# Performance work log

Measured on AMD Instinct MI355X. Metric: run time of the kernel, lower is better.

## Reference

```python
import jax, jax.numpy as jnp
import numpy as np

TEMPERATURE = 0.1
NORM_EPS = 1e-12   # F.normalize default eps
LOSS_EPS = 1e-6

def _l2norm_c(x):
    # L2-normalize along channel dim (axis=1), matching F.normalize(dim=1)
    n = jnp.sqrt(jnp.sum(x * x, axis=1, keepdims=True))
    return x / jnp.maximum(n, NORM_EPS)

def setup_inputs() -> dict:
    key = jax.random.key(0)
    k1, k2, k3 = jax.random.split(key, 3)
    N, C, H, W = 8, 64, 64, 64
    rgb_map = jax.random.normal(k1, (N, C, H, W), dtype=jnp.float32)
    ir_map = jax.random.normal(k2, (N, C, H, W), dtype=jnp.float32)
    targets = jax.random.randint(k3, (N,), 0, 2)  # unused by the forward math
    return {"rgb_map": rgb_map, "ir_map": ir_map, "targets": targets}

def reference(rgb_map, ir_map, targets):
    N, C, H, W = rgb_map.shape
    rgb = _l2norm_c(rgb_map).reshape(N, C, H * W)   # [N, C, P]
    ir = _l2norm_c(ir_map).reshape(N, C, H * W)     # [N, C, P]
    # [N, P, P] similarity, then temperature exp
    logit = jnp.exp(jnp.einsum('ncp,ncq->npq', rgb, ir) / TEMPERATURE)
    pos = jnp.trace(logit, axis1=1, axis2=2)        # diagonal (positive) sum per sample
    tot = jnp.sum(logit, axis=(-1, -2))             # full row/col sum per sample
    loss = -jnp.log(pos / (tot + LOSS_EPS)).mean()
    return loss
```

## Files before the change

kernel.cpp:

```cpp
#include <hip/hip_runtime.h>

#define N_ 8
#define C_ 64
#define P_ 4096

typedef float f32x4 __attribute__((ext_vector_type(4)));
typedef short bf16x8 __attribute__((ext_vector_type(8)));

__device__ __forceinline__ unsigned short f2bf(float f) {
  unsigned int u = __builtin_bit_cast(unsigned int, f);
  u = (u + 0x7fffu + ((u >> 16) & 1u)) >> 16;
  return (unsigned short)u;
}

__global__ void __launch_bounds__(256) norm_transpose(
    const float* __restrict__ rgb, const float* __restrict__ ir,
    unsigned short* __restrict__ rgbnT, unsigned short* __restrict__ irnT) {
  const int idx = blockIdx.x * 256 + threadIdx.x;
  const int n = idx >> 12;
  const int p = idx & (P_ - 1);
  const float* src = (blockIdx.y == 0) ? rgb : ir;
  unsigned short* dst = (blockIdx.y == 0) ? rgbnT : irnT;
  const float SC = 14.4269504088896340736f;
  const float* col = src + (size_t)n * C_ * P_ + p;
  float v[C_];
  float ss = 0.f;
#pragma unroll
  for (int c = 0; c < C_; ++c) {
    v[c] = col[(size_t)c * P_];
    ss += v[c] * v[c];
  }
  float inv = 1.0f / fmaxf(sqrtf(ss), 1e-12f);
  if (blockIdx.y == 0) inv *= SC;
  const int gx = (blockIdx.y == 0) ? 0 : (p & 7);
  unsigned short* o = dst + ((size_t)n * P_ + p) * C_;
#pragma unroll
  for (int g = 0; g < 8; ++g) {
    bf16x8 pack;
#pragma unroll
    for (int j = 0; j < 8; ++j) pack[j] = (short)f2bf(v[g * 8 + j] * inv);
    *reinterpret_cast<bf16x8*>(o + (g ^ gx) * 8) = pack;
  }
}

__device__ __forceinline__ void stage_tile(const unsigned short* src,
                                           unsigned short* dst, int tid,
                                           int wid) {
#pragma unroll
  for (int r = 0; r < 2; ++r) {
    __builtin_amdgcn_global_load_lds(
        (const __attribute__((address_space(1))) void*)(src +
                                                        (size_t)(r * 256 + tid) * 8),
        (__attribute__((address_space(3))) void*)(dst + (r * 256 + wid * 64) * 8),
        16, 0, 0);
  }
}

__global__ void __launch_bounds__(256) gemm_exp_reduce(
    const unsigned short* __restrict__ aT, const unsigned short* __restrict__ bT,
    float* __restrict__ partials) {
  const int lin = blockIdx.x;
  const int n = lin & 7;
  const int local = lin >> 3;
  const int pc = local & 15;
  const int qc = local >> 4;
  const int tid = threadIdx.x;
  const int lane = tid & 63;
  const int wid = tid >> 6;
  const int pbase = pc * 256 + wid * 64;
  const int q0 = qc * 512;
  const unsigned short* A = aT + (size_t)n * P_ * C_;
  const unsigned short* B = bT + (size_t)n * P_ * C_;
  const int r16 = lane & 15;
  const int kofs = (lane >> 4) * 8;

  __shared__ __align__(16) unsigned short bs0[64 * 64];
  __shared__ __align__(16) unsigned short bs1[64 * 64];
  __shared__ __align__(16) unsigned short bs2[64 * 64];
  __shared__ __align__(16) unsigned short bs3[64 * 64];

  bf16x8 af[2][4];
#pragma unroll
  for (int ks = 0; ks < 2; ++ks)
#pragma unroll
    for (int mi = 0; mi < 4; ++mi)
      af[ks][mi] = *reinterpret_cast<const bf16x8*>(
          A + (size_t)(pbase + mi * 16 + r16) * C_ + ks * 32 + kofs);

  stage_tile(B + (size_t)(q0 + 0 * 64) * C_, bs0, tid, wid);
  stage_tile(B + (size_t)(q0 + 1 * 64) * C_, bs1, tid, wid);
  stage_tile(B + (size_t)(q0 + 2 * 64) * C_, bs2, tid, wid);

  unsigned short *pcur = bs0, *pnx1 = bs1, *pnx2 = bs2, *pnx3 = bs3;

  const f32x4 zc = (f32x4)(0.f);
  float t0 = 0.f, t1 = 0.f, t2 = 0.f, t3 = 0.f, pos = 0.f;
  const int col = lane & 15;
  const int rowb = (lane >> 4) * 4;

  unsigned fragoff[2][4];
#pragma unroll
  for (int ks = 0; ks < 2; ++ks)
#pragma unroll
    for (int ni = 0; ni < 4; ++ni) {
      const int row = ni * 16 + r16;
      const int seg = ks * 4 + (lane >> 4);
      fragoff[ks][ni] = (unsigned)((row * 64 + ((seg ^ (lane & 7)) * 8)) * 2);
    }

#pragma unroll 1
  for (int t = 0; t < 8; ++t) {
    asm volatile("s_waitcnt vmcnt(4)" ::: "memory");
    __builtin_amdgcn_sched_barrier(0);
    __builtin_amdgcn_s_barrier();

    int s = t + 3;
    if (s >= 8) s -= 8;
    stage_tile(B + (size_t)(q0 + s * 64) * C_, pnx3, tid, wid);

    const unsigned bpa = (unsigned)(size_t)pcur;
    f32x4 braw[2][4];
#pragma unroll
    for (int ks = 0; ks < 2; ++ks)
#pragma unroll
      for (int ni = 0; ni < 4; ++ni) {
        const unsigned addr = bpa + fragoff[ks][ni];
        asm volatile("ds_read_b128 %0, %1"
                     : "=v"(braw[ks][ni])
                     : "v"(addr));
      }
    asm volatile("s_waitcnt lgkmcnt(0)" ::: "memory");
    __builtin_amdgcn_sched_barrier(0);

    f32x4 acc[4][4];
    __builtin_amdgcn_s_setprio(1);
#pragma unroll
    for (int mi = 0; mi < 4; ++mi)
#pragma unroll
      for (int ni = 0; ni < 4; ++ni)
        acc[mi][ni] = __builtin_amdgcn_mfma_f32_16x16x32_bf16(
            af[0][mi], __builtin_bit_cast(bf16x8, braw[0][ni]), zc, 0, 0, 0);
#pragma unroll
    for (int mi = 0; mi < 4; ++mi)
#pragma unroll
      for (int ni = 0; ni < 4; ++ni)
        acc[mi][ni] = __builtin_amdgcn_mfma_f32_16x16x32_bf16(
            af[1][mi], __builtin_bit_cast(bf16x8, braw[1][ni]), acc[mi][ni],
            0, 0, 0);
    __builtin_amdgcn_s_setprio(0);

#pragma unroll
    for (int mi = 0; mi < 4; ++mi)
#pragma unroll
      for (int ni = 0; ni < 4; ++ni) {
        const f32x4 v = acc[mi][ni];
        t0 += __builtin_amdgcn_exp2f(v[0]);
        t1 += __builtin_amdgcn_exp2f(v[1]);
        t2 += __builtin_amdgcn_exp2f(v[2]);
        t3 += __builtin_amdgcn_exp2f(v[3]);
      }
    const int qb = q0 + t * 64;
    if (pbase == qb) {
#pragma unroll
      for (int mi = 0; mi < 4; ++mi)
#pragma unroll
        for (int r = 0; r < 4; ++r)
          if (rowb + r == col) pos += __builtin_amdgcn_exp2f(acc[mi][mi][r]);
    }

    unsigned short* tmp = pcur;
    pcur = pnx1;
    pnx1 = pnx2;
    pnx2 = pnx3;
    pnx3 = tmp;
  }

  float tot = (t0 + t1) + (t2 + t3);
#pragma unroll
  for (int off = 32; off > 0; off >>= 1) {
    tot += __shfl_down(tot, off);
    pos += __shfl_down(pos, off);
  }
  __shared__ float sb[8];
  if (lane == 0) { sb[wid * 2] = pos; sb[wid * 2 + 1] = tot; }
  __syncthreads();
  if (tid == 0) {
    const float pp = sb[0] + sb[2] + sb[4] + sb[6];
    const float tt = sb[1] + sb[3] + sb[5] + sb[7];
    const int bid = n * 128 + pc * 8 + qc;
    partials[bid * 2] = pp;
    partials[bid * 2 + 1] = tt;
  }
}

__global__ void __launch_bounds__(1024) finalize(
    const float* __restrict__ partials, float* __restrict__ out) {
  const int tid = threadIdx.x;
  const int lane = tid & 63, wid = tid >> 6;
  __shared__ float sp[16], st[16], sl[8];
  const int n = tid >> 7;
  const int i = tid & 127;
  float p = partials[(n * 128 + i) * 2];
  float t = partials[(n * 128 + i) * 2 + 1];
#pragma unroll
  for (int off = 32; off > 0; off >>= 1) {
    p += __shfl_down(p, off);
    t += __shfl_down(t, off);
  }
  if (lane == 0) { sp[wid] = p; st[wid] = t; }
  __syncthreads();
  if (tid < 8) {
    const float pp = sp[2 * tid] + sp[2 * tid + 1];
    const float tt = st[2 * tid] + st[2 * tid + 1];
    sl[tid] = -logf(pp / (tt + 1e-6f));
  }
  __syncthreads();
  if (tid == 0) {
    float loss = 0.f;
#pragma unroll
    for (int k = 0; k < 8; ++k) loss += sl[k];
    out[0] = loss * (1.0f / N_);
  }
}

extern "C" void kernel_launch(void* const* d_in, const int* in_sizes, int n_in,
                              void* d_out, int out_size, void* d_ws, size_t ws_size,
                              hipStream_t stream) {
  const float* rgb = (const float*)d_in[0];
  const float* ir = (const float*)d_in[1];
  float* out = (float*)d_out;

  unsigned short* rgbnT = (unsigned short*)d_ws;
  unsigned short* irnT = rgbnT + (size_t)N_ * P_ * C_;
  float* partials = (float*)(irnT + (size_t)N_ * P_ * C_);

  dim3 g1(N_ * P_ / 256, 2);
  norm_transpose<<<g1, 256, 0, stream>>>(rgb, ir, rgbnT, irnT);

  gemm_exp_reduce<<<1024, 256, 0, stream>>>(rgbnT, irnT, partials);

  finalize<<<1, 1024, 0, stream>>>(partials, out);
}
```

Measured before the change: 41.47 us.

## Give each wave private double-buffered B tiles and drop block barriers

Each wave now stages its own copy of every 64-row B tile into a private double buffer in LDS, so the per-iteration block-wide s_barrier and the shared 4-deep ring are removed. The next tile's load is issued into the current buffer right after its fragments are read into registers. Each wave also writes its own partial sums, which removes the final shared-memory reduction and __syncthreads, and finalize sums four times as many partials. The cost is four times the global/L2 traffic for B and twice the LDS footprint, with only a 2-deep prefetch.

```diff
diff --git a/kernel.cpp b/kernel.cpp
--- a/kernel.cpp
+++ b/kernel.cpp
@@ -43,16 +43,15 @@
   }
 }
 
-__device__ __forceinline__ void stage_tile(const unsigned short* src,
-                                           unsigned short* dst, int tid,
-                                           int wid) {
-#pragma unroll
-  for (int r = 0; r < 2; ++r) {
+__device__ __forceinline__ void stage_tile_wave(const unsigned short* src,
+                                                unsigned short* dst,
+                                                int lane) {
+#pragma unroll
+  for (int r = 0; r < 8; ++r) {
     __builtin_amdgcn_global_load_lds(
         (const __attribute__((address_space(1))) void*)(src +
-                                                        (size_t)(r * 256 + tid) * 8),
-        (__attribute__((address_space(3))) void*)(dst + (r * 256 + wid * 64) * 8),
-        16, 0, 0);
+                                                        (size_t)(r * 64 + lane) * 8),
+        (__attribute__((address_space(3))) void*)(dst + r * 64 * 8), 16, 0, 0);
   }
 }
 
@@ -74,10 +73,7 @@
   const int r16 = lane & 15;
   const int kofs = (lane >> 4) * 8;
 
-  __shared__ __align__(16) unsigned short bs0[64 * 64];
-  __shared__ __align__(16) unsigned short bs1[64 * 64];
-  __shared__ __align__(16) unsigned short bs2[64 * 64];
-  __shared__ __align__(16) unsigned short bs3[64 * 64];
+  __shared__ __align__(16) unsigned short bs[4][2][64 * 64];
 
   bf16x8 af[2][4];
 #pragma unroll
@@ -87,11 +83,11 @@
       af[ks][mi] = *reinterpret_cast<const bf16x8*>(
           A + (size_t)(pbase + mi * 16 + r16) * C_ + ks * 32 + kofs);
 
-  stage_tile(B + (size_t)(q0 + 0 * 64) * C_, bs0, tid, wid);
-  stage_tile(B + (size_t)(q0 + 1 * 64) * C_, bs1, tid, wid);
-  stage_tile(B + (size_t)(q0 + 2 * 64) * C_, bs2, tid, wid);
-
-  unsigned short *pcur = bs0, *pnx1 = bs1, *pnx2 = bs2, *pnx3 = bs3;
+  unsigned short* rb0 = bs[wid][0];
+  unsigned short* rb1 = bs[wid][1];
+
+  stage_tile_wave(B + (size_t)(q0 + 0 * 64) * C_, rb0, lane);
+  stage_tile_wave(B + (size_t)(q0 + 1 * 64) * C_, rb1, lane);
 
   const f32x4 zc = (f32x4)(0.f);
   float t0 = 0.f, t1 = 0.f, t2 = 0.f, t3 = 0.f, pos = 0.f;
@@ -108,15 +104,12 @@
       fragoff[ks][ni] = (unsigned)((row * 64 + ((seg ^ (lane & 7)) * 8)) * 2);
     }
 
+  unsigned short *pcur = rb0, *pnxt = rb1;
+
 #pragma unroll 1
   for (int t = 0; t < 8; ++t) {
-    asm volatile("s_waitcnt vmcnt(4)" ::: "memory");
+    asm volatile("s_waitcnt vmcnt(8)" ::: "memory");
     __builtin_amdgcn_sched_barrier(0);
-    __builtin_amdgcn_s_barrier();
-
-    int s = t + 3;
-    if (s >= 8) s -= 8;
-    stage_tile(B + (size_t)(q0 + s * 64) * C_, pnx3, tid, wid);
 
     const unsigned bpa = (unsigned)(size_t)pcur;
     f32x4 braw[2][4];
@@ -125,12 +118,14 @@
 #pragma unroll
       for (int ni = 0; ni < 4; ++ni) {
         const unsigned addr = bpa + fragoff[ks][ni];
-        asm volatile("ds_read_b128 %0, %1"
-                     : "=v"(braw[ks][ni])
-                     : "v"(addr));
+        asm volatile("ds_read_b128 %0, %1" : "=v"(braw[ks][ni]) : "v"(addr));
       }
     asm volatile("s_waitcnt lgkmcnt(0)" ::: "memory");
     __builtin_amdgcn_sched_barrier(0);
+
+    int s = t + 2;
+    if (s >= 8) s -= 8;
+    stage_tile_wave(B + (size_t)(q0 + s * 64) * C_, pcur, lane);
 
     f32x4 acc[4][4];
     __builtin_amdgcn_s_setprio(1);
@@ -169,10 +164,8 @@
     }
 
     unsigned short* tmp = pcur;
-    pcur = pnx1;
-    pnx1 = pnx2;
-    pnx2 = pnx3;
-    pnx3 = tmp;
+    pcur = pnxt;
+    pnxt = tmp;
   }
 
   float tot = (t0 + t1) + (t2 + t3);
@@ -181,15 +174,10 @@
     tot += __shfl_down(tot, off);
     pos += __shfl_down(pos, off);
   }
-  __shared__ float sb[8];
-  if (lane == 0) { sb[wid * 2] = pos; sb[wid * 2 + 1] = tot; }
-  __syncthreads();
-  if (tid == 0) {
-    const float pp = sb[0] + sb[2] + sb[4] + sb[6];
-    const float tt = sb[1] + sb[3] + sb[5] + sb[7];
-    const int bid = n * 128 + pc * 8 + qc;
-    partials[bid * 2] = pp;
-    partials[bid * 2 + 1] = tt;
+  if (lane == 0) {
+    const int bid = (n * 128 + pc * 8 + qc) * 4 + wid;
+    partials[bid * 2] = pos;
+    partials[bid * 2 + 1] = tot;
   }
 }
 
@@ -200,8 +188,12 @@
   __shared__ float sp[16], st[16], sl[8];
   const int n = tid >> 7;
   const int i = tid & 127;
-  float p = partials[(n * 128 + i) * 2];
-  float t = partials[(n * 128 + i) * 2 + 1];
+  float p = 0.f, t = 0.f;
+#pragma unroll
+  for (int k = 0; k < 4; ++k) {
+    p += partials[(n * 512 + k * 128 + i) * 2];
+    t += partials[(n * 512 + k * 128 + i) * 2 + 1];
+  }
 #pragma unroll
   for (int off = 32; off > 0; off >>= 1) {
     p += __shfl_down(p, off);
```

Measured after the change: 43.16 us. +4.1%, slower.
